# Kernel optimization log

Measured on AMD Instinct MI355X. Metric: run time of the kernel, lower is better.

## Reference

```python
import jax, jax.numpy as jnp
import numpy as np

N_BUS = 200000; N_GEN = 50000
E_BB = 1600000; E_GB = 400000; E_BG = 400000
D_IN = 64; H = 32
OUT_BUS = 4; OUT_GEN = 2


def setup_inputs() -> dict:
    key = jax.random.key(0)
    it = iter(jax.random.split(key, 48))
    def nrm(shape, s=0.05):
        return jax.random.normal(next(it), shape, jnp.float32) * s
    inp = {}
    inp["x_bus"] = jax.random.normal(next(it), (N_BUS, D_IN), jnp.float32)
    inp["x_gen"] = jax.random.normal(next(it), (N_GEN, D_IN), jnp.float32)
    inp["src_bb"] = jax.random.randint(next(it), (E_BB,), 0, N_BUS)
    inp["dst_bb"] = jax.random.randint(next(it), (E_BB,), 0, N_BUS)
    inp["src_gb"] = jax.random.randint(next(it), (E_GB,), 0, N_GEN)
    inp["dst_gb"] = jax.random.randint(next(it), (E_GB,), 0, N_BUS)
    inp["src_bg"] = jax.random.randint(next(it), (E_BG,), 0, N_BUS)
    inp["dst_bg"] = jax.random.randint(next(it), (E_BG,), 0, N_GEN)
    # SAGEConv params per layer / relation: lin_l (on aggregated neighbors, with bias),
    # lin_r (root weight on x_dst, no bias) -- matches PyG SAGEConv defaults.
    for lname, din in (("l1", D_IN), ("l2", H)):
        for rel in ("bb", "gb", "bg"):
            inp[f"{lname}_{rel}_Wl"] = nrm((din, H))
            inp[f"{lname}_{rel}_bl"] = jnp.zeros((H,), jnp.float32)
            inp[f"{lname}_{rel}_Wr"] = nrm((din, H))
    for nt, dout in (("bus", OUT_BUS), ("gen", OUT_GEN)):
        inp[f"lin0_{nt}_W"] = nrm((H, H))
        inp[f"lin0_{nt}_b"] = jnp.zeros((H,), jnp.float32)
        inp[f"linf_{nt}_W"] = nrm((H, dout))
        inp[f"linf_{nt}_b"] = jnp.zeros((dout,), jnp.float32)
    return inp


def _sage(x_src, x_dst, src, dst, Wl, bl, Wr, n_dst):
    # SAGEConv: mean-aggregate neighbor features, then out = lin_l(mean) + lin_r(x_dst)
    msg = jax.ops.segment_sum(x_src[src], dst, num_segments=n_dst)
    cnt = jax.ops.segment_sum(jnp.ones((src.shape[0],), x_src.dtype), dst, num_segments=n_dst)
    mean = msg / jnp.maximum(cnt, 1.0)[:, None]
    return mean @ Wl + bl + x_dst @ Wr


def reference(x_bus, x_gen, src_bb, dst_bb, src_gb, dst_gb, src_bg, dst_bg,
              l1_bb_Wl, l1_bb_bl, l1_bb_Wr, l1_gb_Wl, l1_gb_bl, l1_gb_Wr,
              l1_bg_Wl, l1_bg_bl, l1_bg_Wr,
              l2_bb_Wl, l2_bb_bl, l2_bb_Wr, l2_gb_Wl, l2_gb_bl, l2_gb_Wr,
              l2_bg_Wl, l2_bg_bl, l2_bg_Wr,
              lin0_bus_W, lin0_bus_b, lin0_gen_W, lin0_gen_b,
              linf_bus_W, linf_bus_b, linf_gen_W, linf_gen_b):
    # HeteroConv layer 1 (aggr='sum' over relations targeting each dst type)
    hb = (_sage(x_bus, x_bus, src_bb, dst_bb, l1_bb_Wl, l1_bb_bl, l1_bb_Wr, N_BUS)
          + _sage(x_gen, x_bus, src_gb, dst_gb, l1_gb_Wl, l1_gb_bl, l1_gb_Wr, N_BUS))
    hg = _sage(x_bus, x_gen, src_bg, dst_bg, l1_bg_Wl, l1_bg_bl, l1_bg_Wr, N_GEN)
    xb, xg = jax.nn.relu(hb), jax.nn.relu(hg)  # dropout is identity in eval mode
    # HeteroConv layer 2
    hb = (_sage(xb, xb, src_bb, dst_bb, l2_bb_Wl, l2_bb_bl, l2_bb_Wr, N_BUS)
          + _sage(xg, xb, src_gb, dst_gb, l2_gb_Wl, l2_gb_bl, l2_gb_Wr, N_BUS))
    hg = _sage(xb, xg, src_bg, dst_bg, l2_bg_Wl, l2_bg_bl, l2_bg_Wr, N_GEN)
    xb, xg = jax.nn.relu(hb), jax.nn.relu(hg)
    # per-node-type hidden Linear (input relu'd again as in the original; relu is idempotent)
    xb = jax.nn.relu(xb) @ lin0_bus_W + lin0_bus_b
    xg = jax.nn.relu(xg) @ lin0_gen_W + lin0_gen_b
    out_bus = xb @ linf_bus_W + linf_bus_b
    out_gen = xg @ linf_gen_W + linf_gen_b
    return out_bus, out_gen
```

## Files before the change

kernel.cpp:

```cpp
#include <hip/hip_runtime.h>
#include <hip/hip_bf16.h>

#define N_BUS 200000
#define N_GEN 50000
#define E_BB 1600000
#define E_GB 400000
#define E_BG 400000
#define H 32
#define NBINS 1024
#define EPT 16

#define NBK_BUS 782
#define NBK_GEN 196
#define CAP_BB 2560
#define CAP_GB 768
#define CAP_BG 2560

#define NB_PART_BB 391
#define NB_PART_GB 98
#define NB_PART_BG 98
#define NB_PART_ALL 587
#define NB_TF_BUS 782
#define NB_TF_GEN 196
#define NB_PL_BUS 6250
#define NB_PL_GEN 1563

typedef __attribute__((ext_vector_type(8))) short short8;
typedef __attribute__((ext_vector_type(4))) float floatx4;

__device__ inline unsigned short f2bf(float f) {
    __hip_bfloat16 h = __float2bfloat16(f);
    return *reinterpret_cast<unsigned short*>(&h);
}
__device__ inline float bf2f(unsigned short u) {
    return __uint_as_float(((unsigned)u) << 16);
}

__device__ __forceinline__ void part_body(int blk, const int* __restrict__ src,
                                          const int* __restrict__ dst, int nE,
                                          unsigned* __restrict__ cnt_g, int CAP,
                                          unsigned* __restrict__ pairs) {
    __shared__ unsigned hist[NBINS];
    __shared__ unsigned base[NBINS];
    __shared__ unsigned sbase[NBINS];
    __shared__ unsigned sh[256];
    __shared__ unsigned pairv[256 * EPT];
    __shared__ unsigned short bid[256 * EPT];
    const int tid = threadIdx.x;
    const int cbase = blk * (256 * EPT);
    const int total = min(256 * EPT, nE - cbase);

    unsigned es[EPT], ed[EPT];
#pragma unroll
    for (int q = 0; q < EPT; q++) {
        int i = cbase + q * 256 + tid;
        if (i < nE) { es[q] = (unsigned)src[i]; ed[q] = (unsigned)dst[i]; }
        else ed[q] = 0xFFFFFFFFu;
    }
    for (int i = tid; i < NBINS; i += 256) hist[i] = 0;
    __syncthreads();
#pragma unroll
    for (int q = 0; q < EPT; q++)
        if (ed[q] != 0xFFFFFFFFu) atomicAdd(&hist[ed[q] >> 8], 1u);
    __syncthreads();

    unsigned h4[4];
    unsigned s = 0;
#pragma unroll
    for (int k2 = 0; k2 < 4; k2++) { h4[k2] = hist[tid * 4 + k2]; s += h4[k2]; }
    sh[tid] = s;
    __syncthreads();
#pragma unroll
    for (int d = 1; d < 256; d <<= 1) {
        unsigned t = (tid >= d) ? sh[tid - d] : 0u;
        __syncthreads();
        sh[tid] += t;
        __syncthreads();
    }
    unsigned run = sh[tid] - s;
#pragma unroll
    for (int k2 = 0; k2 < 4; k2++) {
        int b = tid * 4 + k2;
        sbase[b] = run;
        base[b] = h4[k2] ? ((unsigned)b * CAP + atomicAdd(&cnt_g[b], h4[k2])) : 0u;
        hist[b] = 0;
        run += h4[k2];
    }
    __syncthreads();

#pragma unroll
    for (int q = 0; q < EPT; q++) {
        if (ed[q] != 0xFFFFFFFFu) {
            unsigned b = ed[q] >> 8;
            unsigned off = atomicAdd(&hist[b], 1u);
            unsigned p = sbase[b] + off;
            pairv[p] = ((ed[q] & 255u) << 24) | es[q];
            bid[p] = (unsigned short)b;
        }
    }
    __syncthreads();

    for (int p = tid; p < total; p += 256) {
        unsigned b = bid[p];
        pairs[base[b] + ((unsigned)p - sbase[b])] = pairv[p];
    }
}

__global__ __launch_bounds__(256) void part_all_kernel(
    const int* __restrict__ sbb, const int* __restrict__ dbb, unsigned* __restrict__ cbb, unsigned* __restrict__ pbb,
    const int* __restrict__ sgb, const int* __restrict__ dgb, unsigned* __restrict__ cgb, unsigned* __restrict__ pgb,
    const int* __restrict__ sbg, const int* __restrict__ dbg, unsigned* __restrict__ cbg, unsigned* __restrict__ pbg)
{
    int b = blockIdx.x;
    if (b < NB_PART_BB) part_body(b, sbb, dbb, E_BB, cbb, CAP_BB, pbb);
    else if (b < NB_PART_BB + NB_PART_GB) part_body(b - NB_PART_BB, sgb, dgb, E_GB, cgb, CAP_GB, pgb);
    else part_body(b - NB_PART_BB - NB_PART_GB, sbg, dbg, E_BG, cbg, CAP_BG, pbg);
}

__device__ __forceinline__ void fine_body(int b, const unsigned* __restrict__ cnt_g, int CAP,
                                          const unsigned* __restrict__ pairs,
                                          unsigned* __restrict__ rs,
                                          unsigned* __restrict__ esrc, int nDst) {
    __shared__ unsigned cnt[256];
    __shared__ unsigned sh[256];
    __shared__ unsigned stg[2560];
    const int tid = threadIdx.x;
    const unsigned start = (unsigned)b * CAP;
    const unsigned m = cnt_g[b];
    const unsigned end = start + m;

    cnt[tid] = 0;
    __syncthreads();
    for (unsigned k = start + tid; k < end; k += 256)
        atomicAdd(&cnt[pairs[k] >> 24], 1u);
    __syncthreads();
    unsigned c = cnt[tid];
    sh[tid] = c;
    __syncthreads();
#pragma unroll
    for (int d = 1; d < 256; d <<= 1) {
        unsigned t = (tid >= d) ? sh[tid - d] : 0u;
        __syncthreads();
        sh[tid] += t;
        __syncthreads();
    }
    int gd = b * 256 + tid;
    unsigned rowstart = start + sh[tid] - c;
    if (gd < nDst) rs[gd] = (rowstart << 9) | (c < 511u ? c : 511u);
    cnt[tid] = sh[tid] - c;
    __syncthreads();
    for (unsigned k = start + tid; k < end; k += 256) {
        unsigned p = pairs[k];
        unsigned off = atomicAdd(&cnt[p >> 24], 1u);
        stg[off] = p & 0x00FFFFFFu;
    }
    __syncthreads();
    for (unsigned p = tid; p < m; p += 256) esrc[start + p] = stg[p];
}

__global__ __launch_bounds__(256) void fine_all_kernel(
    const unsigned* __restrict__ cbb, const unsigned* __restrict__ pbb, unsigned* __restrict__ rsbb, unsigned* __restrict__ ebb,
    const unsigned* __restrict__ cgb, const unsigned* __restrict__ pgb, unsigned* __restrict__ rsgb, unsigned* __restrict__ egb,
    const unsigned* __restrict__ cbg, const unsigned* __restrict__ pbg, unsigned* __restrict__ rsbg, unsigned* __restrict__ ebg)
{
    int b = blockIdx.x;
    if (b < NBK_BUS) fine_body(b, cbb, CAP_BB, pbb, rsbb, ebb, N_BUS);
    else if (b < 2 * NBK_BUS) fine_body(b - NBK_BUS, cgb, CAP_GB, pgb, rsgb, egb, N_BUS);
    else fine_body(b - 2 * NBK_BUS, cbg, CAP_BG, pbg, rsbg, ebg, N_GEN);
}

__global__ __launch_bounds__(256) void prep_kernel(
    const float* __restrict__ l1_bb_Wl, const float* __restrict__ l1_bb_bl, const float* __restrict__ l1_bb_Wr,
    const float* __restrict__ l1_gb_Wl, const float* __restrict__ l1_gb_bl, const float* __restrict__ l1_gb_Wr,
    const float* __restrict__ l1_bg_Wl, const float* __restrict__ l1_bg_bl, const float* __restrict__ l1_bg_Wr,
    const float* __restrict__ l2_bb_Wl, const float* __restrict__ l2_bb_bl, const float* __restrict__ l2_bb_Wr,
    const float* __restrict__ l2_gb_Wl, const float* __restrict__ l2_gb_bl, const float* __restrict__ l2_gb_Wr,
    const float* __restrict__ l2_bg_Wl, const float* __restrict__ l2_bg_bl, const float* __restrict__ l2_bg_Wr,
    const float* __restrict__ lin0_bus_W, const float* __restrict__ lin0_bus_b,
    const float* __restrict__ linf_bus_W, const float* __restrict__ linf_bus_b,
    const float* __restrict__ lin0_gen_W, const float* __restrict__ lin0_gen_b,
    const float* __restrict__ linf_gen_W, const float* __restrict__ linf_gen_b,
    unsigned short* __restrict__ Wf1b, float* __restrict__ B1b,
    unsigned short* __restrict__ Wf1g, float* __restrict__ B1g,
    unsigned short* __restrict__ Wf2b, float* __restrict__ B2b,
    unsigned short* __restrict__ Wf2g, float* __restrict__ B2g,
    float* __restrict__ WeB, float* __restrict__ beB,
    float* __restrict__ WeG, float* __restrict__ beG,
    unsigned* __restrict__ cursors)
{
    int t0 = blockIdx.x * 256 + threadIdx.x;
    int NT = gridDim.x * 256;

    if (t0 < 3 * NBINS) cursors[t0] = 0u;

    for (int f = t0; f < 2 * 6 * 64 * 8; f += NT) {
        int j = f & 7, l = (f >> 3) & 63, tile = f >> 9;
        int nt = tile % 6, kt = tile / 6;
        int k = kt * 32 + (l >> 4) * 8 + j, n = nt * 16 + (l & 15);
        float v;
        if (n < 32) v = l1_bb_Wl[k * 32 + n];
        else if (n < 64) v = l1_bg_Wl[k * 32 + n - 32];
        else v = l1_bb_Wr[k * 32 + n - 64] + l1_gb_Wr[k * 32 + n - 64];
        Wf1b[f] = f2bf(v);
    }
    for (int f = t0; f < 2 * 4 * 64 * 8; f += NT) {
        int j = f & 7, l = (f >> 3) & 63, tile = f >> 9;
        int nt = tile % 4, kt = tile / 4;
        int k = kt * 32 + (l >> 4) * 8 + j, n = nt * 16 + (l & 15);
        float v = (n < 32) ? l1_gb_Wl[k * 32 + n] : l1_bg_Wr[k * 32 + n - 32];
        Wf1g[f] = f2bf(v);
    }
    for (int f = t0; f < 6 * 64 * 8; f += NT) {
        int j = f & 7, l = (f >> 3) & 63, nt = f >> 9;
        int k = (l >> 4) * 8 + j, n = nt * 16 + (l & 15);
        float v;
        if (n < 32) v = l2_bb_Wl[k * 32 + n];
        else if (n < 64) v = l2_bg_Wl[k * 32 + n - 32];
        else v = l2_bb_Wr[k * 32 + n - 64] + l2_gb_Wr[k * 32 + n - 64];
        Wf2b[f] = f2bf(v);
    }
    for (int f = t0; f < 4 * 64 * 8; f += NT) {
        int j = f & 7, l = (f >> 3) & 63, nt = f >> 9;
        int k = (l >> 4) * 8 + j, n = nt * 16 + (l & 15);
        float v = (n < 32) ? l2_gb_Wl[k * 32 + n] : l2_bg_Wr[k * 32 + n - 32];
        Wf2g[f] = f2bf(v);
    }
    if (t0 < 96) {
        B1b[t0] = (t0 < 64) ? 0.0f : l1_bb_bl[t0 - 64] + l1_gb_bl[t0 - 64];
        B2b[t0] = (t0 < 64) ? 0.0f : l2_bb_bl[t0 - 64] + l2_gb_bl[t0 - 64];
    }
    if (t0 < 64) {
        B1g[t0] = (t0 < 32) ? 0.0f : l1_bg_bl[t0 - 32];
        B2g[t0] = (t0 < 32) ? 0.0f : l2_bg_bl[t0 - 32];
    }
    if (t0 < 128) {
        int k = t0 >> 2, c = t0 & 3;
        float s = 0.0f;
        for (int m = 0; m < 32; m++) s += lin0_bus_W[k * 32 + m] * linf_bus_W[m * 4 + c];
        WeB[t0] = s;
    }
    if (t0 >= 128 && t0 < 132) {
        int c = t0 - 128;
        float s = linf_bus_b[c];
        for (int m = 0; m < 32; m++) s += lin0_bus_b[m] * linf_bus_W[m * 4 + c];
        beB[c] = s;
    }
    if (t0 >= 132 && t0 < 196) {
        int i = t0 - 132, k = i >> 1, c = i & 1;
        float s = 0.0f;
        for (int m = 0; m < 32; m++) s += lin0_gen_W[k * 32 + m] * linf_gen_W[m * 2 + c];
        WeG[i] = s;
    }
    if (t0 >= 196 && t0 < 198) {
        int c = t0 - 196;
        float s = linf_gen_b[c];
        for (int m = 0; m < 32; m++) s += lin0_gen_b[m] * linf_gen_W[m * 2 + c];
        beG[c] = s;
    }
}

template <int K, int NOUT>
__device__ __forceinline__ void mfma_tail(
    int rows, int base,
    const unsigned short* __restrict__ Wf, const float* __restrict__ bias,
    unsigned short* __restrict__ y0, unsigned short* __restrict__ y1, float* __restrict__ h,
    char* ldsraw)
{
    constexpr int KT = K / 32, NTN = NOUT / 16, NCH = NOUT / 32;
    constexpr int XS = K + 8;
    constexpr int OS = 34;
    short* lx = (short*)ldsraw;
    float* lo = (float*)ldsraw;
    const int tid = threadIdx.x;
    const int w = tid >> 6, l = tid & 63, quad = l >> 4, ln = l & 15;

    short8 bf[KT][NTN];
    const short8* wf8 = (const short8*)Wf;
#pragma unroll
    for (int kt = 0; kt < KT; kt++)
#pragma unroll
        for (int nt = 0; nt < NTN; nt++)
            bf[kt][nt] = wf8[(kt * NTN + nt) * 64 + l];
    float bv[NTN];
#pragma unroll
    for (int nt = 0; nt < NTN; nt++) bv[nt] = bias[nt * 16 + ln];

    floatx4 acc[4][NTN];
#pragma unroll
    for (int mt = 0; mt < 4; mt++)
#pragma unroll
        for (int nt = 0; nt < NTN; nt++) {
            floatx4 c0 = {bv[nt], bv[nt], bv[nt], bv[nt]};
            acc[mt][nt] = c0;
        }
#pragma unroll
    for (int mt = 0; mt < 4; mt++) {
        const int row = w * 64 + mt * 16 + ln;
#pragma unroll
        for (int kt = 0; kt < KT; kt++) {
            short8 af = *(const short8*)&lx[row * XS + kt * 32 + quad * 8];
#pragma unroll
            for (int nt = 0; nt < NTN; nt++)
                acc[mt][nt] = __builtin_amdgcn_mfma_f32_16x16x32_bf16(
                    af, bf[kt][nt], acc[mt][nt], 0, 0, 0);
        }
    }

#pragma unroll
    for (int c = 0; c < NCH; c++) {
        __syncthreads();
#pragma unroll
        for (int mt = 0; mt < 4; mt++)
#pragma unroll
            for (int d = 0; d < 2; d++) {
                int nt = 2 * c + d;
#pragma unroll
                for (int r = 0; r < 4; r++)
                    lo[(w * 64 + mt * 16 + quad * 4 + r) * OS + d * 16 + ln] = acc[mt][nt][r];
            }
        __syncthreads();
        const int T4 = rows * 8;
        if (c == NCH - 1) {
            float* og = h + (size_t)base * 32;
            for (int q = tid; q < T4; q += 256) {
                int r = q >> 3, cc = (q & 7) * 4;
                const float* p = &lo[r * OS + cc];
                *(float4*)(og + q * 4) = make_float4(p[0], p[1], p[2], p[3]);
            }
        } else {
            unsigned short* og = ((c == 0) ? y0 : y1) + (size_t)base * 32;
            for (int q = tid; q < T4; q += 256) {
                int r = q >> 3, cc = (q & 7) * 4;
                const float* p = &lo[r * OS + cc];
                short4 s4;
                s4.x = (short)f2bf(p[0]); s4.y = (short)f2bf(p[1]);
                s4.z = (short)f2bf(p[2]); s4.w = (short)f2bf(p[3]);
                *(short4*)(og + q * 4) = s4;
            }
        }
    }
}

template <int K, int NOUT>
__device__ __forceinline__ void transform_body(
    int blk, const float* x, int n,
    const unsigned short* __restrict__ Wf, const float* __restrict__ bias,
    unsigned short* __restrict__ y0, unsigned short* __restrict__ y1, float* h,
    char* ldsraw)
{
    constexpr int XS = K + 8;
    short* lx = (short*)ldsraw;
    const int tid = threadIdx.x;
    const int base = blk * 256;
    const int rows = min(256, n - base);

    {
        const float4* xg = (const float4*)(x + (size_t)base * K);
        const int T4 = rows * (K / 4);
        for (int q = tid; q < T4; q += 256) {
            float4 v = xg[q];
            int r = q / (K / 4), c = (q % (K / 4)) * 4;
            short4 s4;
            s4.x = (short)f2bf(v.x); s4.y = (short)f2bf(v.y);
            s4.z = (short)f2bf(v.z); s4.w = (short)f2bf(v.w);
            *(short4*)&lx[r * XS + c] = s4;
        }
    }
    __syncthreads();
    mfma_tail<K, NOUT>(rows, base, Wf, bias, y0, y1, h, ldsraw);
}

template <int NOUT>
__device__ __forceinline__ void transform_bf16_body(
    int blk, const unsigned short* x, int n,
    const unsigned short* __restrict__ Wf, const float* __restrict__ bias,
    unsigned short* __restrict__ y0, unsigned short* __restrict__ y1, float* h,
    char* ldsraw)
{
    constexpr int K = 32, XS = K + 8;
    short* lx = (short*)ldsraw;
    const int tid = threadIdx.x;
    const int base = blk * 256;
    const int rows = min(256, n - base);

    {
        const short8* xg = (const short8*)(x + (size_t)base * K);
        const int T8 = rows * (K / 8);
        for (int q = tid; q < T8; q += 256) {
            short8 v = xg[q];
            int r = q / (K / 8), c = (q % (K / 8)) * 8;
            *(short8*)&lx[r * XS + c] = v;
        }
    }
    __syncthreads();
    mfma_tail<K, NOUT>(rows, base, Wf, bias, y0, y1, h, ldsraw);
}

__global__ __launch_bounds__(256) void tf1_all_kernel(
    const float* xb, const unsigned short* __restrict__ Wfb, const float* __restrict__ Bb,
    unsigned short* __restrict__ yb0, unsigned short* __restrict__ yb1, float* hb,
    const float* xg, const unsigned short* __restrict__ Wfg, const float* __restrict__ Bg,
    unsigned short* __restrict__ yg0, float* hg)
{
    constexpr int XB = 256 * (64 + 8) * 2, OB = 256 * 34 * 4;
    __shared__ __align__(16) char ldsraw[(XB > OB) ? XB : OB];
    int b = blockIdx.x;
    if (b < NB_TF_BUS)
        transform_body<64, 96>(b, xb, N_BUS, Wfb, Bb, yb0, yb1, hb, ldsraw);
    else
        transform_body<64, 64>(b - NB_TF_BUS, xg, N_GEN, Wfg, Bg, yg0, nullptr, hg, ldsraw);
}

__global__ __launch_bounds__(256) void tf2b_all_kernel(
    const unsigned short* x2b, const unsigned short* __restrict__ Wfb, const float* __restrict__ Bb,
    unsigned short* __restrict__ yb0, unsigned short* __restrict__ yb1, float* hb,
    const unsigned short* x2g, const unsigned short* __restrict__ Wfg, const float* __restrict__ Bg,
    unsigned short* __restrict__ yg0, float* hg)
{
    constexpr int XB = 256 * (32 + 8) * 2, OB = 256 * 34 * 4;
    __shared__ __align__(16) char ldsraw[(XB > OB) ? XB : OB];
    int b = blockIdx.x;
    if (b < NB_TF_BUS)
        transform_bf16_body<96>(b, x2b, N_BUS, Wfb, Bb, yb0, yb1, hb, ldsraw);
    else
        transform_bf16_body<64>(b - NB_TF_BUS, x2g, N_GEN, Wfg, Bg, yg0, nullptr, hg, ldsraw);
}

__device__ __forceinline__ void agg_one(
    unsigned u, const unsigned* __restrict__ e,
    const unsigned short* __restrict__ y, int j, float4& r)
{
    unsigned k0 = u >> 9;
    unsigned c = u & 511u;
    unsigned k1 = k0 + c;
    float4 a0 = make_float4(0.f, 0.f, 0.f, 0.f);
    float4 a1 = a0, a2 = a0, a3 = a0;
    unsigned k = k0;
    if (k + 4 <= k1) {
        unsigned s0 = e[k], s1 = e[k + 1], s2 = e[k + 2], s3 = e[k + 3];
        for (; k + 8 <= k1; k += 4) {
            unsigned t0 = e[k + 4], t1 = e[k + 5], t2 = e[k + 6], t3 = e[k + 7];
            ushort4 v0 = *(const ushort4*)(y + (size_t)s0 * H + j);
            ushort4 v1 = *(const ushort4*)(y + (size_t)s1 * H + j);
            ushort4 v2 = *(const ushort4*)(y + (size_t)s2 * H + j);
            ushort4 v3 = *(const ushort4*)(y + (size_t)s3 * H + j);
            a0.x += bf2f(v0.x); a0.y += bf2f(v0.y); a0.z += bf2f(v0.z); a0.w += bf2f(v0.w);
            a1.x += bf2f(v1.x); a1.y += bf2f(v1.y); a1.z += bf2f(v1.z); a1.w += bf2f(v1.w);
            a2.x += bf2f(v2.x); a2.y += bf2f(v2.y); a2.z += bf2f(v2.z); a2.w += bf2f(v2.w);
            a3.x += bf2f(v3.x); a3.y += bf2f(v3.y); a3.z += bf2f(v3.z); a3.w += bf2f(v3.w);
            s0 = t0; s1 = t1; s2 = t2; s3 = t3;
        }
        {
            ushort4 v0 = *(const ushort4*)(y + (size_t)s0 * H + j);
            ushort4 v1 = *(const ushort4*)(y + (size_t)s1 * H + j);
            ushort4 v2 = *(const ushort4*)(y + (size_t)s2 * H + j);
            ushort4 v3 = *(const ushort4*)(y + (size_t)s3 * H + j);
            a0.x += bf2f(v0.x); a0.y += bf2f(v0.y); a0.z += bf2f(v0.z); a0.w += bf2f(v0.w);
            a1.x += bf2f(v1.x); a1.y += bf2f(v1.y); a1.z += bf2f(v1.z); a1.w += bf2f(v1.w);
            a2.x += bf2f(v2.x); a2.y += bf2f(v2.y); a2.z += bf2f(v2.z); a2.w += bf2f(v2.w);
            a3.x += bf2f(v3.x); a3.y += bf2f(v3.y); a3.z += bf2f(v3.z); a3.w += bf2f(v3.w);
            k += 4;
        }
    }
    for (; k < k1; ++k) {
        unsigned s = e[k];
        const ushort4 v = *(const ushort4*)(y + (size_t)s * H + j);
        a0.x += bf2f(v.x); a0.y += bf2f(v.y); a0.z += bf2f(v.z); a0.w += bf2f(v.w);
    }
    a0.x += a1.x + a2.x + a3.x; a0.y += a1.y + a2.y + a3.y;
    a0.z += a1.z + a2.z + a3.z; a0.w += a1.w + a2.w + a3.w;
    float inv = 1.0f / (float)(c > 1u ? c : 1u);
    r.x += a0.x * inv; r.y += a0.y * inv; r.z += a0.z * inv; r.w += a0.w * inv;
}

template <bool FUSE>
__device__ __forceinline__ void pull_body(
    int blk, bool hasB, int n,
    const unsigned* __restrict__ rsA, const unsigned* __restrict__ eA, const unsigned short* __restrict__ yA,
    const unsigned* __restrict__ rsB, const unsigned* __restrict__ eB, const unsigned short* __restrict__ yB,
    const float* __restrict__ h, unsigned short* __restrict__ x2,
    const float* __restrict__ We, const float* __restrict__ be, int DOUT, float* __restrict__ outp)
{
    const int tid = threadIdx.x;
    unsigned node = blk * 32u + (tid >> 3);
    int j = (tid & 7) * 4;
    if (node >= (unsigned)n) return;

    float4 r = *(const float4*)(h + (size_t)node * H + j);

    agg_one(rsA[node], eA, yA, j, r);
    if (hasB) agg_one(rsB[node], eB, yB, j, r);

    if (!FUSE) {
        ushort4 o;
        o.x = f2bf(fmaxf(r.x, 0.f)); o.y = f2bf(fmaxf(r.y, 0.f));
        o.z = f2bf(fmaxf(r.z, 0.f)); o.w = f2bf(fmaxf(r.w, 0.f));
        *(ushort4*)(x2 + (size_t)node * H + j) = o;
        return;
    }

    float p0 = fmaxf(r.x, 0.f), p1 = fmaxf(r.y, 0.f), p2 = fmaxf(r.z, 0.f), p3 = fmaxf(r.w, 0.f);
    float tot[4];
#pragma unroll
    for (int c = 0; c < 4; c++) {
        if (c < DOUT) {
            tot[c] = p0 * We[(j + 0) * DOUT + c] + p1 * We[(j + 1) * DOUT + c]
                   + p2 * We[(j + 2) * DOUT + c] + p3 * We[(j + 3) * DOUT + c];
        } else tot[c] = 0.f;
    }
#pragma unroll
    for (int mask = 1; mask <= 4; mask <<= 1) {
#pragma unroll
        for (int c = 0; c < 4; c++) tot[c] += __shfl_xor(tot[c], mask);
    }
    if ((tid & 7) == 0) {
        if (DOUT == 4) {
            *(float4*)(outp + (size_t)node * 4) =
                make_float4(tot[0] + be[0], tot[1] + be[1], tot[2] + be[2], tot[3] + be[3]);
        } else {
            *(float2*)(outp + (size_t)node * 2) = make_float2(tot[0] + be[0], tot[1] + be[1]);
        }
    }
}

template <bool FUSE>
__global__ __launch_bounds__(256) void pull_all_kernel(
    const unsigned* __restrict__ rsbb, const unsigned* __restrict__ ebb, const unsigned short* __restrict__ ybb,
    const unsigned* __restrict__ rsgb, const unsigned* __restrict__ egb, const unsigned short* __restrict__ ygb,
    const float* __restrict__ hb, unsigned short* __restrict__ x2b,
    const float* __restrict__ WeB, const float* __restrict__ beB,
    const unsigned* __restrict__ rsbg, const unsigned* __restrict__ ebg, const unsigned short* __restrict__ ybg,
    const float* __restrict__ hg, unsigned short* __restrict__ x2g,
    const float* __restrict__ WeG, const float* __restrict__ beG,
    float* __restrict__ outp)
{
    int b = blockIdx.x;
    if (b < NB_PL_BUS)
        pull_body<FUSE>(b, true, N_BUS, rsbb, ebb, ybb, rsgb, egb, ygb, hb, x2b, WeB, beB, 4, outp);
    else
        pull_body<FUSE>(b - NB_PL_BUS, false, N_GEN, rsbg, ebg, ybg, nullptr, nullptr, nullptr,
                        hg, x2g, WeG, beG, 2, outp ? outp + (size_t)N_BUS * 4 : nullptr);
}

extern "C" void kernel_launch(void* const* d_in, const int* in_sizes, int n_in,
                              void* d_out, int out_size, void* d_ws, size_t ws_size,
                              hipStream_t stream) {
    const float* x_bus = (const float*)d_in[0];
    const float* x_gen = (const float*)d_in[1];
    const int* src_bb = (const int*)d_in[2];
    const int* dst_bb = (const int*)d_in[3];
    const int* src_gb = (const int*)d_in[4];
    const int* dst_gb = (const int*)d_in[5];
    const int* src_bg = (const int*)d_in[6];
    const int* dst_bg = (const int*)d_in[7];
    const float* l1_bb_Wl = (const float*)d_in[8];
    const float* l1_bb_bl = (const float*)d_in[9];
    const float* l1_bb_Wr = (const float*)d_in[10];
    const float* l1_gb_Wl = (const float*)d_in[11];
    const float* l1_gb_bl = (const float*)d_in[12];
    const float* l1_gb_Wr = (const float*)d_in[13];
    const float* l1_bg_Wl = (const float*)d_in[14];
    const float* l1_bg_bl = (const float*)d_in[15];
    const float* l1_bg_Wr = (const float*)d_in[16];
    const float* l2_bb_Wl = (const float*)d_in[17];
    const float* l2_bb_bl = (const float*)d_in[18];
    const float* l2_bb_Wr = (const float*)d_in[19];
    const float* l2_gb_Wl = (const float*)d_in[20];
    const float* l2_gb_bl = (const float*)d_in[21];
    const float* l2_gb_Wr = (const float*)d_in[22];
    const float* l2_bg_Wl = (const float*)d_in[23];
    const float* l2_bg_bl = (const float*)d_in[24];
    const float* l2_bg_Wr = (const float*)d_in[25];
    const float* lin0_bus_W = (const float*)d_in[26];
    const float* lin0_bus_b = (const float*)d_in[27];
    const float* linf_bus_W = (const float*)d_in[28];
    const float* linf_bus_b = (const float*)d_in[29];
    const float* lin0_gen_W = (const float*)d_in[30];
    const float* lin0_gen_b = (const float*)d_in[31];
    const float* linf_gen_W = (const float*)d_in[32];
    const float* linf_gen_b = (const float*)d_in[33];

    char* ws = (char*)d_ws;
    size_t off = 0;
    auto alloc = [&](size_t bytes) {
        char* p = ws + off;
        off += (bytes + 255) & ~(size_t)255;
        return p;
    };
    unsigned* rs_bb = (unsigned*)alloc((size_t)N_BUS * 4);
    unsigned* rs_gb = (unsigned*)alloc((size_t)N_BUS * 4);
    unsigned* rs_bg = (unsigned*)alloc((size_t)N_GEN * 4);
    unsigned* cur_bb = (unsigned*)alloc(NBINS * 4);
    unsigned* cur_gb = (unsigned*)alloc(NBINS * 4);
    unsigned* cur_bg = (unsigned*)alloc(NBINS * 4);
    unsigned* e_bb = (unsigned*)alloc((size_t)NBK_BUS * CAP_BB * 4);
    unsigned* e_gb = (unsigned*)alloc((size_t)NBK_BUS * CAP_GB * 4);
    unsigned* e_bg = (unsigned*)alloc((size_t)NBK_GEN * CAP_BG * 4);
    unsigned* p_bb = (unsigned*)alloc((size_t)NBK_BUS * CAP_BB * 4);
    unsigned* p_gb = (unsigned*)alloc((size_t)NBK_BUS * CAP_GB * 4);
    unsigned* p_bg = (unsigned*)alloc((size_t)NBK_GEN * CAP_BG * 4);
    unsigned short* y_bb = (unsigned short*)alloc((size_t)N_BUS * H * 2);
    unsigned short* y_bg = (unsigned short*)alloc((size_t)N_BUS * H * 2);
    unsigned short* y_gb = (unsigned short*)alloc((size_t)N_GEN * H * 2);
    float* h_bus = (float*)alloc((size_t)N_BUS * H * 4);
    float* h_gen = (float*)alloc((size_t)N_GEN * H * 4);
    unsigned short* x2_bus = (unsigned short*)alloc((size_t)N_BUS * H * 2);
    unsigned short* x2_gen = (unsigned short*)alloc((size_t)N_GEN * H * 2);
    unsigned short* Wf1b = (unsigned short*)alloc(2 * 6 * 64 * 8 * 2);
    float* B1b = (float*)alloc(96 * 4);
    unsigned short* Wf1g = (unsigned short*)alloc(2 * 4 * 64 * 8 * 2);
    float* B1g = (float*)alloc(64 * 4);
    unsigned short* Wf2b = (unsigned short*)alloc(6 * 64 * 8 * 2);
    float* B2b = (float*)alloc(96 * 4);
    unsigned short* Wf2g = (unsigned short*)alloc(4 * 64 * 8 * 2);
    float* B2g = (float*)alloc(64 * 4);
    float* WeB = (float*)alloc(128 * 4);
    float* beB = (float*)alloc(4 * 4);
    float* WeG = (float*)alloc(64 * 4);
    float* beG = (float*)alloc(2 * 4);

    prep_kernel<<<32, 256, 0, stream>>>(
        l1_bb_Wl, l1_bb_bl, l1_bb_Wr, l1_gb_Wl, l1_gb_bl, l1_gb_Wr,
        l1_bg_Wl, l1_bg_bl, l1_bg_Wr, l2_bb_Wl, l2_bb_bl, l2_bb_Wr,
        l2_gb_Wl, l2_gb_bl, l2_gb_Wr, l2_bg_Wl, l2_bg_bl, l2_bg_Wr,
        lin0_bus_W, lin0_bus_b, linf_bus_W, linf_bus_b,
        lin0_gen_W, lin0_gen_b, linf_gen_W, linf_gen_b,
        Wf1b, B1b, Wf1g, B1g, Wf2b, B2b, Wf2g, B2g, WeB, beB, WeG, beG,
        cur_bb);

    part_all_kernel<<<NB_PART_ALL, 256, 0, stream>>>(
        src_bb, dst_bb, cur_bb, p_bb, src_gb, dst_gb, cur_gb, p_gb, src_bg, dst_bg, cur_bg, p_bg);

    fine_all_kernel<<<2 * NBK_BUS + NBK_GEN, 256, 0, stream>>>(
        cur_bb, p_bb, rs_bb, e_bb, cur_gb, p_gb, rs_gb, e_gb, cur_bg, p_bg, rs_bg, e_bg);

    tf1_all_kernel<<<NB_TF_BUS + NB_TF_GEN, 256, 0, stream>>>(
        x_bus, Wf1b, B1b, y_bb, y_bg, h_bus, x_gen, Wf1g, B1g, y_gb, h_gen);

    pull_all_kernel<false><<<NB_PL_BUS + NB_PL_GEN, 256, 0, stream>>>(
        rs_bb, e_bb, y_bb, rs_gb, e_gb, y_gb, h_bus, x2_bus, WeB, beB,
        rs_bg, e_bg, y_bg, h_gen, x2_gen, WeG, beG, nullptr);

    tf2b_all_kernel<<<NB_TF_BUS + NB_TF_GEN, 256, 0, stream>>>(
        x2_bus, Wf2b, B2b, y_bb, y_bg, h_bus, x2_gen, Wf2g, B2g, y_gb, h_gen);

    pull_all_kernel<true><<<NB_PL_BUS + NB_PL_GEN, 256, 0, stream>>>(
        rs_bb, e_bb, y_bb, rs_gb, e_gb, y_gb, h_bus, nullptr, WeB, beB,
        rs_bg, e_bg, y_bg, h_gen, nullptr, WeG, beG, (float*)d_out);
}
```

Baseline: 351.7 us.

## Aggregate from coarse-binned pairs with LDS atomics and fuse into transforms

Drops the fine CSR-building pass. Each 256-node block now reads its coarse-bin pairs directly, counts degrees in LDS and accumulates the scaled neighbor features into an LDS accumulator with shared-memory atomics. The layer-1 aggregation is fused with the layer-2 MFMA transform, and the layer-2 aggregation is fused with the output head, cutting the kernel count and the intermediate x2, rs and esrc round-trips through global memory. The trade-off is heavy LDS float atomic contention, less parallelism per block (one block per 256 nodes instead of 32), and an accumulation order that is no longer deterministic.

```diff
diff --git a/kernel.cpp b/kernel.cpp
--- a/kernel.cpp
+++ b/kernel.cpp
@@ -22,8 +22,9 @@
 #define NB_PART_ALL 587
 #define NB_TF_BUS 782
 #define NB_TF_GEN 196
-#define NB_PL_BUS 6250
-#define NB_PL_GEN 1563
+
+#define M24 0x00FFFFFFu
+#define PNONE 0xFFFFFFFFu
 
 typedef __attribute__((ext_vector_type(8))) short short8;
 typedef __attribute__((ext_vector_type(4))) float floatx4;
@@ -55,13 +56,13 @@
     for (int q = 0; q < EPT; q++) {
         int i = cbase + q * 256 + tid;
         if (i < nE) { es[q] = (unsigned)src[i]; ed[q] = (unsigned)dst[i]; }
-        else ed[q] = 0xFFFFFFFFu;
+        else ed[q] = PNONE;
     }
     for (int i = tid; i < NBINS; i += 256) hist[i] = 0;
     __syncthreads();
 #pragma unroll
     for (int q = 0; q < EPT; q++)
-        if (ed[q] != 0xFFFFFFFFu) atomicAdd(&hist[ed[q] >> 8], 1u);
+        if (ed[q] != PNONE) atomicAdd(&hist[ed[q] >> 8], 1u);
     __syncthreads();
 
     unsigned h4[4];
@@ -90,7 +91,7 @@
 
 #pragma unroll
     for (int q = 0; q < EPT; q++) {
-        if (ed[q] != 0xFFFFFFFFu) {
+        if (ed[q] != PNONE) {
             unsigned b = ed[q] >> 8;
             unsigned off = atomicAdd(&hist[b], 1u);
             unsigned p = sbase[b] + off;
@@ -115,58 +116,6 @@
     if (b < NB_PART_BB) part_body(b, sbb, dbb, E_BB, cbb, CAP_BB, pbb);
     else if (b < NB_PART_BB + NB_PART_GB) part_body(b - NB_PART_BB, sgb, dgb, E_GB, cgb, CAP_GB, pgb);
     else part_body(b - NB_PART_BB - NB_PART_GB, sbg, dbg, E_BG, cbg, CAP_BG, pbg);
-}
-
-__device__ __forceinline__ void fine_body(int b, const unsigned* __restrict__ cnt_g, int CAP,
-                                          const unsigned* __restrict__ pairs,
-                                          unsigned* __restrict__ rs,
-                                          unsigned* __restrict__ esrc, int nDst) {
-    __shared__ unsigned cnt[256];
-    __shared__ unsigned sh[256];
-    __shared__ unsigned stg[2560];
-    const int tid = threadIdx.x;
-    const unsigned start = (unsigned)b * CAP;
-    const unsigned m = cnt_g[b];
-    const unsigned end = start + m;
-
-    cnt[tid] = 0;
-    __syncthreads();
-    for (unsigned k = start + tid; k < end; k += 256)
-        atomicAdd(&cnt[pairs[k] >> 24], 1u);
-    __syncthreads();
-    unsigned c = cnt[tid];
-    sh[tid] = c;
-    __syncthreads();
-#pragma unroll
-    for (int d = 1; d < 256; d <<= 1) {
-        unsigned t = (tid >= d) ? sh[tid - d] : 0u;
-        __syncthreads();
-        sh[tid] += t;
-        __syncthreads();
-    }
-    int gd = b * 256 + tid;
-    unsigned rowstart = start + sh[tid] - c;
-    if (gd < nDst) rs[gd] = (rowstart << 9) | (c < 511u ? c : 511u);
-    cnt[tid] = sh[tid] - c;
-    __syncthreads();
-    for (unsigned k = start + tid; k < end; k += 256) {
-        unsigned p = pairs[k];
-        unsigned off = atomicAdd(&cnt[p >> 24], 1u);
-        stg[off] = p & 0x00FFFFFFu;
-    }
-    __syncthreads();
-    for (unsigned p = tid; p < m; p += 256) esrc[start + p] = stg[p];
-}
-
-__global__ __launch_bounds__(256) void fine_all_kernel(
-    const unsigned* __restrict__ cbb, const unsigned* __restrict__ pbb, unsigned* __restrict__ rsbb, unsigned* __restrict__ ebb,
-    const unsigned* __restrict__ cgb, const unsigned* __restrict__ pgb, unsigned* __restrict__ rsgb, unsigned* __restrict__ egb,
-    const unsigned* __restrict__ cbg, const unsigned* __restrict__ pbg, unsigned* __restrict__ rsbg, unsigned* __restrict__ ebg)
-{
-    int b = blockIdx.x;
-    if (b < NBK_BUS) fine_body(b, cbb, CAP_BB, pbb, rsbb, ebb, N_BUS);
-    else if (b < 2 * NBK_BUS) fine_body(b - NBK_BUS, cgb, CAP_GB, pgb, rsgb, egb, N_BUS);
-    else fine_body(b - 2 * NBK_BUS, cbg, CAP_BG, pbg, rsbg, ebg, N_GEN);
 }
 
 __global__ __launch_bounds__(256) void prep_kernel(
@@ -259,18 +208,15 @@
     }
 }
 
-template <int K, int NOUT>
+template <int K, int NOUT, int XS>
 __device__ __forceinline__ void mfma_tail(
     int rows, int base,
     const unsigned short* __restrict__ Wf, const float* __restrict__ bias,
     unsigned short* __restrict__ y0, unsigned short* __restrict__ y1, float* __restrict__ h,
-    char* ldsraw)
+    short* lx, float* lo)
 {
     constexpr int KT = K / 32, NTN = NOUT / 16, NCH = NOUT / 32;
-    constexpr int XS = K + 8;
     constexpr int OS = 34;
-    short* lx = (short*)ldsraw;
-    float* lo = (float*)ldsraw;
     const int tid = threadIdx.x;
     const int w = tid >> 6, l = tid & 63, quad = l >> 4, ln = l & 15;
 
@@ -367,33 +313,7 @@
         }
     }
     __syncthreads();
-    mfma_tail<K, NOUT>(rows, base, Wf, bias, y0, y1, h, ldsraw);
-}
-
-template <int NOUT>
-__device__ __forceinline__ void transform_bf16_body(
-    int blk, const unsigned short* x, int n,
-    const unsigned short* __restrict__ Wf, const float* __restrict__ bias,
-    unsigned short* __restrict__ y0, unsigned short* __restrict__ y1, float* h,
-    char* ldsraw)
-{
-    constexpr int K = 32, XS = K + 8;
-    short* lx = (short*)ldsraw;
-    const int tid = threadIdx.x;
-    const int base = blk * 256;
-    const int rows = min(256, n - base);
-
-    {
-        const short8* xg = (const short8*)(x + (size_t)base * K);
-        const int T8 = rows * (K / 8);
-        for (int q = tid; q < T8; q += 256) {
-            short8 v = xg[q];
-            int r = q / (K / 8), c = (q % (K / 8)) * 8;
-            *(short8*)&lx[r * XS + c] = v;
-        }
-    }
-    __syncthreads();
-    mfma_tail<K, NOUT>(rows, base, Wf, bias, y0, y1, h, ldsraw);
+    mfma_tail<K, NOUT, XS>(rows, base, Wf, bias, y0, y1, h, (short*)ldsraw, (float*)ldsraw);
 }
 
 __global__ __launch_bounds__(256) void tf1_all_kernel(
@@ -411,135 +331,222 @@
         transform_body<64, 64>(b - NB_TF_BUS, xg, N_GEN, Wfg, Bg, yg0, nullptr, hg, ldsraw);
 }
 
-__global__ __launch_bounds__(256) void tf2b_all_kernel(
-    const unsigned short* x2b, const unsigned short* __restrict__ Wfb, const float* __restrict__ Bb,
-    unsigned short* __restrict__ yb0, unsigned short* __restrict__ yb1, float* hb,
-    const unsigned short* x2g, const unsigned short* __restrict__ Wfg, const float* __restrict__ Bg,
-    unsigned short* __restrict__ yg0, float* hg)
-{
-    constexpr int XB = 256 * (32 + 8) * 2, OB = 256 * 34 * 4;
-    __shared__ __align__(16) char ldsraw[(XB > OB) ? XB : OB];
+__device__ __forceinline__ void agg_accum(
+    const unsigned* __restrict__ pairs, unsigned m,
+    const unsigned short* __restrict__ y,
+    const float* __restrict__ inv, float* __restrict__ hacc,
+    int g, int jc)
+{
+    unsigned pA = (unsigned)g, pB = (unsigned)g + 64u;
+    unsigned prA = (pA < m) ? pairs[pA] : PNONE;
+    unsigned prB = (pB < m) ? pairs[pB] : PNONE;
+    while (prA != PNONE || prB != PNONE) {
+        short8 vA, vB;
+        float ivA = 0.f, ivB = 0.f;
+        unsigned ldA = 0, ldB = 0;
+        bool hA = (prA != PNONE), hB = (prB != PNONE);
+        if (hA) {
+            ldA = prA >> 24;
+            vA = *(const short8*)(y + (size_t)(prA & M24) * H + jc);
+            ivA = inv[ldA];
+        }
+        if (hB) {
+            ldB = prB >> 24;
+            vB = *(const short8*)(y + (size_t)(prB & M24) * H + jc);
+            ivB = inv[ldB];
+        }
+        pA += 128u; pB += 128u;
+        prA = (pA < m) ? pairs[pA] : PNONE;
+        prB = (pB < m) ? pairs[pB] : PNONE;
+        if (hA) {
+            float* hb = &hacc[ldA * H + jc];
+#pragma unroll
+            for (int k = 0; k < 8; k++)
+                atomicAdd(&hb[k], bf2f((unsigned short)vA[k]) * ivA);
+        }
+        if (hB) {
+            float* hb = &hacc[ldB * H + jc];
+#pragma unroll
+            for (int k = 0; k < 8; k++)
+                atomicAdd(&hb[k], bf2f((unsigned short)vB[k]) * ivB);
+        }
+    }
+}
+
+template <bool HASB>
+__device__ __forceinline__ void agg_prologue(
+    int base, int rows,
+    const unsigned* __restrict__ pairsA, unsigned mA, const unsigned short* __restrict__ yA,
+    const unsigned* __restrict__ pairsB, unsigned mB, const unsigned short* __restrict__ yB,
+    const float* __restrict__ hroot,
+    float* hacc, unsigned* degA, unsigned* degB)
+{
+    const int tid = threadIdx.x;
+    float* invA = (float*)degA;
+    float* invB = (float*)degB;
+
+    degA[tid] = 0u;
+    if (HASB) degB[tid] = 0u;
+    {
+        const float4* g4 = (const float4*)(hroot + (size_t)base * H);
+        const int R4 = rows * 8;
+        for (int i = tid; i < 256 * 8; i += 256) {
+            float4 v = (i < R4) ? g4[i] : make_float4(0.f, 0.f, 0.f, 0.f);
+            *(float4*)&hacc[i * 4] = v;
+        }
+    }
+    __syncthreads();
+    for (unsigned p = tid; p < mA; p += 256) atomicAdd(&degA[pairsA[p] >> 24], 1u);
+    if (HASB)
+        for (unsigned p = tid; p < mB; p += 256) atomicAdd(&degB[pairsB[p] >> 24], 1u);
+    __syncthreads();
+    {
+        unsigned dA = degA[tid];
+        invA[tid] = 1.0f / (float)(dA > 1u ? dA : 1u);
+        if (HASB) {
+            unsigned dB = degB[tid];
+            invB[tid] = 1.0f / (float)(dB > 1u ? dB : 1u);
+        }
+    }
+    __syncthreads();
+    const int g = tid >> 2;
+    const int jc = (tid & 3) * 8;
+    agg_accum(pairsA, mA, yA, invA, hacc, g, jc);
+    if (HASB) agg_accum(pairsB, mB, yB, invB, hacc, g, jc);
+    __syncthreads();
+}
+
+template <int NOUT, bool HASB>
+__device__ __forceinline__ void aggtf_body(
+    int blk, int n,
+    const unsigned* __restrict__ pairsA, unsigned mA, const unsigned short* __restrict__ yA,
+    const unsigned* __restrict__ pairsB, unsigned mB, const unsigned short* __restrict__ yB,
+    float* __restrict__ hroot,
+    const unsigned short* __restrict__ Wf, const float* __restrict__ bias,
+    unsigned short* __restrict__ y0, unsigned short* __restrict__ y1,
+    char* __restrict__ lds)
+{
+    constexpr int XS = 32;
+    float* hacc = (float*)lds;
+    unsigned* degA = (unsigned*)(lds + 32768);
+    unsigned* degB = (unsigned*)(lds + 33792);
+    short* lx = (short*)(lds + 34816);
+    float* lo = (float*)lds;
+    const int tid = threadIdx.x;
+    const int base = blk * 256;
+    const int rows = min(256, n - base);
+
+    agg_prologue<HASB>(base, rows, pairsA, mA, yA, pairsB, mB, yB, hroot,
+                       hacc, degA, degB);
+
+    for (int i = tid; i < 256 * 8; i += 256) {
+        float4 v = *(const float4*)&hacc[i * 4];
+        int r = i >> 3, c4 = (i & 7) * 4;
+        short4 s4;
+        s4.x = (short)f2bf(fmaxf(v.x, 0.f));
+        s4.y = (short)f2bf(fmaxf(v.y, 0.f));
+        s4.z = (short)f2bf(fmaxf(v.z, 0.f));
+        s4.w = (short)f2bf(fmaxf(v.w, 0.f));
+        *(short4*)&lx[r * XS + c4] = s4;
+    }
+    __syncthreads();
+    mfma_tail<32, NOUT, XS>(rows, base, Wf, bias, y0, y1, hroot, lx, lo);
+}
+
+__global__ __launch_bounds__(256, 3) void aggtf2_all_kernel(
+    const unsigned* __restrict__ pbb, const unsigned* __restrict__ cbb, const unsigned short* __restrict__ ybb,
+    const unsigned* __restrict__ pgb, const unsigned* __restrict__ cgb, const unsigned short* __restrict__ ygb,
+    float* __restrict__ hb, const unsigned short* __restrict__ Wfb, const float* __restrict__ Bb,
+    unsigned short* __restrict__ y2bb, unsigned short* __restrict__ y2bg,
+    const unsigned* __restrict__ pbg, const unsigned* __restrict__ cbg, const unsigned short* __restrict__ ybg,
+    float* __restrict__ hg, const unsigned short* __restrict__ Wfg, const float* __restrict__ Bg,
+    unsigned short* __restrict__ y2gb)
+{
+    __shared__ __align__(16) char lds[51200];
     int b = blockIdx.x;
     if (b < NB_TF_BUS)
-        transform_bf16_body<96>(b, x2b, N_BUS, Wfb, Bb, yb0, yb1, hb, ldsraw);
-    else
-        transform_bf16_body<64>(b - NB_TF_BUS, x2g, N_GEN, Wfg, Bg, yg0, nullptr, hg, ldsraw);
-}
-
-__device__ __forceinline__ void agg_one(
-    unsigned u, const unsigned* __restrict__ e,
-    const unsigned short* __restrict__ y, int j, float4& r)
-{
-    unsigned k0 = u >> 9;
-    unsigned c = u & 511u;
-    unsigned k1 = k0 + c;
-    float4 a0 = make_float4(0.f, 0.f, 0.f, 0.f);
-    float4 a1 = a0, a2 = a0, a3 = a0;
-    unsigned k = k0;
-    if (k + 4 <= k1) {
-        unsigned s0 = e[k], s1 = e[k + 1], s2 = e[k + 2], s3 = e[k + 3];
-        for (; k + 8 <= k1; k += 4) {
-            unsigned t0 = e[k + 4], t1 = e[k + 5], t2 = e[k + 6], t3 = e[k + 7];
-            ushort4 v0 = *(const ushort4*)(y + (size_t)s0 * H + j);
-            ushort4 v1 = *(const ushort4*)(y + (size_t)s1 * H + j);
-            ushort4 v2 = *(const ushort4*)(y + (size_t)s2 * H + j);
-            ushort4 v3 = *(const ushort4*)(y + (size_t)s3 * H + j);
-            a0.x += bf2f(v0.x); a0.y += bf2f(v0.y); a0.z += bf2f(v0.z); a0.w += bf2f(v0.w);
-            a1.x += bf2f(v1.x); a1.y += bf2f(v1.y); a1.z += bf2f(v1.z); a1.w += bf2f(v1.w);
-            a2.x += bf2f(v2.x); a2.y += bf2f(v2.y); a2.z += bf2f(v2.z); a2.w += bf2f(v2.w);
-            a3.x += bf2f(v3.x); a3.y += bf2f(v3.y); a3.z += bf2f(v3.z); a3.w += bf2f(v3.w);
-            s0 = t0; s1 = t1; s2 = t2; s3 = t3;
-        }
-        {
-            ushort4 v0 = *(const ushort4*)(y + (size_t)s0 * H + j);
-            ushort4 v1 = *(const ushort4*)(y + (size_t)s1 * H + j);
-            ushort4 v2 = *(const ushort4*)(y + (size_t)s2 * H + j);
-            ushort4 v3 = *(const ushort4*)(y + (size_t)s3 * H + j);
-            a0.x += bf2f(v0.x); a0.y += bf2f(v0.y); a0.z += bf2f(v0.z); a0.w += bf2f(v0.w);
-            a1.x += bf2f(v1.x); a1.y += bf2f(v1.y); a1.z += bf2f(v1.z); a1.w += bf2f(v1.w);
-            a2.x += bf2f(v2.x); a2.y += bf2f(v2.y); a2.z += bf2f(v2.z); a2.w += bf2f(v2.w);
-            a3.x += bf2f(v3.x); a3.y += bf2f(v3.y); a3.z += bf2f(v3.z); a3.w += bf2f(v3.w);
-            k += 4;
-        }
-    }
-    for (; k < k1; ++k) {
-        unsigned s = e[k];
-        const ushort4 v = *(const ushort4*)(y + (size_t)s * H + j);
-        a0.x += bf2f(v.x); a0.y += bf2f(v.y); a0.z += bf2f(v.z); a0.w += bf2f(v.w);
-    }
-    a0.x += a1.x + a2.x + a3.x; a0.y += a1.y + a2.y + a3.y;
-    a0.z += a1.z + a2.z + a3.z; a0.w += a1.w + a2.w + a3.w;
-    float inv = 1.0f / (float)(c > 1u ? c : 1u);
-    r.x += a0.x * inv; r.y += a0.y * inv; r.z += a0.z * inv; r.w += a0.w * inv;
-}
-
-template <bool FUSE>
-__device__ __forceinline__ void pull_body(
-    int blk, bool hasB, int n,
-    const unsigned* __restrict__ rsA, const unsigned* __restrict__ eA, const unsigned short* __restrict__ yA,
-    const unsigned* __restrict__ rsB, const unsigned* __restrict__ eB, const unsigned short* __restrict__ yB,
-    const float* __restrict__ h, unsigned short* __restrict__ x2,
-    const float* __restrict__ We, const float* __restrict__ be, int DOUT, float* __restrict__ outp)
-{
+        aggtf_body<96, true>(b, N_BUS, pbb + (size_t)b * CAP_BB, cbb[b], ybb,
+                             pgb + (size_t)b * CAP_GB, cgb[b], ygb,
+                             hb, Wfb, Bb, y2bb, y2bg, lds);
+    else {
+        int g = b - NB_TF_BUS;
+        aggtf_body<64, false>(g, N_GEN, pbg + (size_t)g * CAP_BG, cbg[g], ybg,
+                              nullptr, 0u, nullptr,
+                              hg, Wfg, Bg, y2gb, nullptr, lds);
+    }
+}
+
+template <bool HASB>
+__device__ __forceinline__ void agghead_body(
+    int blk, int n,
+    const unsigned* __restrict__ pairsA, unsigned mA, const unsigned short* __restrict__ yA,
+    const unsigned* __restrict__ pairsB, unsigned mB, const unsigned short* __restrict__ yB,
+    const float* __restrict__ hroot,
+    const float* __restrict__ We, const float* __restrict__ be, int DOUT,
+    float* __restrict__ outp, char* __restrict__ lds)
+{
+    float* hacc = (float*)lds;
+    unsigned* degA = (unsigned*)(lds + 32768);
+    unsigned* degB = (unsigned*)(lds + 33792);
     const int tid = threadIdx.x;
-    unsigned node = blk * 32u + (tid >> 3);
-    int j = (tid & 7) * 4;
-    if (node >= (unsigned)n) return;
-
-    float4 r = *(const float4*)(h + (size_t)node * H + j);
-
-    agg_one(rsA[node], eA, yA, j, r);
-    if (hasB) agg_one(rsB[node], eB, yB, j, r);
-
-    if (!FUSE) {
-        ushort4 o;
-        o.x = f2bf(fmaxf(r.x, 0.f)); o.y = f2bf(fmaxf(r.y, 0.f));
-        o.z = f2bf(fmaxf(r.z, 0.f)); o.w = f2bf(fmaxf(r.w, 0.f));
-        *(ushort4*)(x2 + (size_t)node * H + j) = o;
-        return;
-    }
-
-    float p0 = fmaxf(r.x, 0.f), p1 = fmaxf(r.y, 0.f), p2 = fmaxf(r.z, 0.f), p3 = fmaxf(r.w, 0.f);
-    float tot[4];
-#pragma unroll
-    for (int c = 0; c < 4; c++) {
-        if (c < DOUT) {
-            tot[c] = p0 * We[(j + 0) * DOUT + c] + p1 * We[(j + 1) * DOUT + c]
-                   + p2 * We[(j + 2) * DOUT + c] + p3 * We[(j + 3) * DOUT + c];
-        } else tot[c] = 0.f;
-    }
-#pragma unroll
-    for (int mask = 1; mask <= 4; mask <<= 1) {
-#pragma unroll
-        for (int c = 0; c < 4; c++) tot[c] += __shfl_xor(tot[c], mask);
-    }
-    if ((tid & 7) == 0) {
-        if (DOUT == 4) {
-            *(float4*)(outp + (size_t)node * 4) =
-                make_float4(tot[0] + be[0], tot[1] + be[1], tot[2] + be[2], tot[3] + be[3]);
-        } else {
-            *(float2*)(outp + (size_t)node * 2) = make_float2(tot[0] + be[0], tot[1] + be[1]);
-        }
-    }
-}
-
-template <bool FUSE>
-__global__ __launch_bounds__(256) void pull_all_kernel(
-    const unsigned* __restrict__ rsbb, const unsigned* __restrict__ ebb, const unsigned short* __restrict__ ybb,
-    const unsigned* __restrict__ rsgb, const unsigned* __restrict__ egb, const unsigned short* __restrict__ ygb,
-    const float* __restrict__ hb, unsigned short* __restrict__ x2b,
-    const float* __restrict__ WeB, const float* __restrict__ beB,
-    const unsigned* __restrict__ rsbg, const unsigned* __restrict__ ebg, const unsigned short* __restrict__ ybg,
-    const float* __restrict__ hg, unsigned short* __restrict__ x2g,
-    const float* __restrict__ WeG, const float* __restrict__ beG,
+    const int base = blk * 256;
+    const int rows = min(256, n - base);
+
+    agg_prologue<HASB>(base, rows, pairsA, mA, yA, pairsB, mB, yB, hroot,
+                       hacc, degA, degB);
+
+    const int lane8 = tid & 7;
+    const int j = lane8 * 4;
+    for (int rr = tid >> 3; rr < 256; rr += 32) {
+        int node = base + rr;
+        bool act = node < n;
+        float4 v = act ? *(const float4*)&hacc[rr * H + j] : make_float4(0.f, 0.f, 0.f, 0.f);
+        float p0 = fmaxf(v.x, 0.f), p1 = fmaxf(v.y, 0.f);
+        float p2 = fmaxf(v.z, 0.f), p3 = fmaxf(v.w, 0.f);
+        float tot[4];
+#pragma unroll
+        for (int c = 0; c < 4; c++) {
+            if (c < DOUT) {
+                tot[c] = p0 * We[(j + 0) * DOUT + c] + p1 * We[(j + 1) * DOUT + c]
+                       + p2 * We[(j + 2) * DOUT + c] + p3 * We[(j + 3) * DOUT + c];
+            } else tot[c] = 0.f;
+        }
+#pragma unroll
+        for (int mask = 1; mask <= 4; mask <<= 1) {
+#pragma unroll
+            for (int c = 0; c < 4; c++) tot[c] += __shfl_xor(tot[c], mask);
+        }
+        if (act && lane8 == 0) {
+            if (DOUT == 4) {
+                *(float4*)(outp + (size_t)node * 4) =
+                    make_float4(tot[0] + be[0], tot[1] + be[1], tot[2] + be[2], tot[3] + be[3]);
+            } else {
+                *(float2*)(outp + (size_t)node * 2) = make_float2(tot[0] + be[0], tot[1] + be[1]);
+            }
+        }
+    }
+}
+
+__global__ __launch_bounds__(256, 4) void agghead_all_kernel(
+    const unsigned* __restrict__ pbb, const unsigned* __restrict__ cbb, const unsigned short* __restrict__ y2bb,
+    const unsigned* __restrict__ pgb, const unsigned* __restrict__ cgb, const unsigned short* __restrict__ y2gb,
+    const float* __restrict__ hb, const float* __restrict__ WeB, const float* __restrict__ beB,
+    const unsigned* __restrict__ pbg, const unsigned* __restrict__ cbg, const unsigned short* __restrict__ y2bg,
+    const float* __restrict__ hg, const float* __restrict__ WeG, const float* __restrict__ beG,
     float* __restrict__ outp)
 {
+    __shared__ __align__(16) char lds[34816];
     int b = blockIdx.x;
-    if (b < NB_PL_BUS)
-        pull_body<FUSE>(b, true, N_BUS, rsbb, ebb, ybb, rsgb, egb, ygb, hb, x2b, WeB, beB, 4, outp);
-    else
-        pull_body<FUSE>(b - NB_PL_BUS, false, N_GEN, rsbg, ebg, ybg, nullptr, nullptr, nullptr,
-                        hg, x2g, WeG, beG, 2, outp ? outp + (size_t)N_BUS * 4 : nullptr);
+    if (b < NB_TF_BUS)
+        agghead_body<true>(b, N_BUS, pbb + (size_t)b * CAP_BB, cbb[b], y2bb,
+                           pgb + (size_t)b * CAP_GB, cgb[b], y2gb,
+                           hb, WeB, beB, 4, outp, lds);
+    else {
+        int g = b - NB_TF_BUS;
+        agghead_body<false>(g, N_GEN, pbg + (size_t)g * CAP_BG, cbg[g], y2bg,
+                            nullptr, 0u, nullptr,
+                            hg, WeG, beG, 2, outp + (size_t)N_BUS * 4, lds);
+    }
 }
 
 extern "C" void kernel_launch(void* const* d_in, const int* in_sizes, int n_in,
@@ -587,25 +594,20 @@
         off += (bytes + 255) & ~(size_t)255;
         return p;
     };
-    unsigned* rs_bb = (unsigned*)alloc((size_t)N_BUS * 4);
-    unsigned* rs_gb = (unsigned*)alloc((size_t)N_BUS * 4);
-    unsigned* rs_bg = (unsigned*)alloc((size_t)N_GEN * 4);
     unsigned* cur_bb = (unsigned*)alloc(NBINS * 4);
     unsigned* cur_gb = (unsigned*)alloc(NBINS * 4);
     unsigned* cur_bg = (unsigned*)alloc(NBINS * 4);
-    unsigned* e_bb = (unsigned*)alloc((size_t)NBK_BUS * CAP_BB * 4);
-    unsigned* e_gb = (unsigned*)alloc((size_t)NBK_BUS * CAP_GB * 4);
-    unsigned* e_bg = (unsigned*)alloc((size_t)NBK_GEN * CAP_BG * 4);
     unsigned* p_bb = (unsigned*)alloc((size_t)NBK_BUS * CAP_BB * 4);
     unsigned* p_gb = (unsigned*)alloc((size_t)NBK_BUS * CAP_GB * 4);
     unsigned* p_bg = (unsigned*)alloc((size_t)NBK_GEN * CAP_BG * 4);
     unsigned short* y_bb = (unsigned short*)alloc((size_t)N_BUS * H * 2);
     unsigned short* y_bg = (unsigned short*)alloc((size_t)N_BUS * H * 2);
     unsigned short* y_gb = (unsigned short*)alloc((size_t)N_GEN * H * 2);
+    unsigned short* y2_bb = (unsigned short*)alloc((size_t)N_BUS * H * 2);
+    unsigned short* y2_bg = (unsigned short*)alloc((size_t)N_BUS * H * 2);
+    unsigned short* y2_gb = (unsigned short*)alloc((size_t)N_GEN * H * 2);
     float* h_bus = (float*)alloc((size_t)N_BUS * H * 4);
     float* h_gen = (float*)alloc((size_t)N_GEN * H * 4);
-    unsigned short* x2_bus = (unsigned short*)alloc((size_t)N_BUS * H * 2);
-    unsigned short* x2_gen = (unsigned short*)alloc((size_t)N_GEN * H * 2);
     unsigned short* Wf1b = (unsigned short*)alloc(2 * 6 * 64 * 8 * 2);
     float* B1b = (float*)alloc(96 * 4);
     unsigned short* Wf1g = (unsigned short*)alloc(2 * 4 * 64 * 8 * 2);
@@ -631,20 +633,14 @@
     part_all_kernel<<<NB_PART_ALL, 256, 0, stream>>>(
         src_bb, dst_bb, cur_bb, p_bb, src_gb, dst_gb, cur_gb, p_gb, src_bg, dst_bg, cur_bg, p_bg);
 
-    fine_all_kernel<<<2 * NBK_BUS + NBK_GEN, 256, 0, stream>>>(
-        cur_bb, p_bb, rs_bb, e_bb, cur_gb, p_gb, rs_gb, e_gb, cur_bg, p_bg, rs_bg, e_bg);
-
     tf1_all_kernel<<<NB_TF_BUS + NB_TF_GEN, 256, 0, stream>>>(
         x_bus, Wf1b, B1b, y_bb, y_bg, h_bus, x_gen, Wf1g, B1g, y_gb, h_gen);
 
-    pull_all_kernel<false><<<NB_PL_BUS + NB_PL_GEN, 256, 0, stream>>>(
-        rs_bb, e_bb, y_bb, rs_gb, e_gb, y_gb, h_bus, x2_bus, WeB, beB,
-        rs_bg, e_bg, y_bg, h_gen, x2_gen, WeG, beG, nullptr);
-
-    tf2b_all_kernel<<<NB_TF_BUS + NB_TF_GEN, 256, 0, stream>>>(
-        x2_bus, Wf2b, B2b, y_bb, y_bg, h_bus, x2_gen, Wf2g, B2g, y_gb, h_gen);
-
-    pull_all_kernel<true><<<NB_PL_BUS + NB_PL_GEN, 256, 0, stream>>>(
-        rs_bb, e_bb, y_bb, rs_gb, e_gb, y_gb, h_bus, nullptr, WeB, beB,
-        rs_bg, e_bg, y_bg, h_gen, nullptr, WeG, beG, (float*)d_out);
-}
+    aggtf2_all_kernel<<<NB_TF_BUS + NB_TF_GEN, 256, 0, stream>>>(
+        p_bb, cur_bb, y_bb, p_gb, cur_gb, y_gb, h_bus, Wf2b, B2b, y2_bb, y2_bg,
+        p_bg, cur_bg, y_bg, h_gen, Wf2g, B2g, y2_gb);
+
+    agghead_all_kernel<<<NB_TF_BUS + NB_TF_GEN, 256, 0, stream>>>(
+        p_bb, cur_bb, y2_bb, p_gb, cur_gb, y2_gb, h_bus, WeB, beB,
+        p_bg, cur_bg, y2_bg, h_gen, WeG, beG, (float*)d_out);
+}
```

Result: slower. 1.099 ms (+212.5%).
